# Performance work log

Measured on AMD Instinct MI355X. Metric: run time of the kernel, lower is better.

## Reference

```python
import jax, jax.numpy as jnp
import numpy as np

N_NODES = 50000
N_EDGES = 800000
IN_C = 128
OUT_C = 128
BN_EPS = 1e-5


def setup_inputs() -> dict:
    key = jax.random.key(0)
    k1, k2, k3 = jax.random.split(key, 3)
    x = jax.random.normal(k1, (N_NODES, IN_C), dtype=jnp.float32)
    edge_index = jax.random.randint(k2, (2, N_EDGES), 0, N_NODES, dtype=jnp.int32)
    W = jax.random.normal(k3, (IN_C, OUT_C), dtype=jnp.float32) * (1.0 / np.sqrt(IN_C))
    bias = jnp.zeros((OUT_C,), dtype=jnp.float32)
    gamma = jnp.ones((OUT_C,), dtype=jnp.float32)
    beta = jnp.zeros((OUT_C,), dtype=jnp.float32)
    return {"x": x, "W": W, "bias": bias, "gamma": gamma, "beta": beta,
            "edge_index": edge_index}


def reference(x, W, bias, gamma, beta, edge_index):
    # GCNConv (PyG defaults): add self-loops, symmetric normalization, linear, scatter-add
    n = x.shape[0]
    h = x @ W  # [N, out_c]
    loops = jnp.arange(n, dtype=edge_index.dtype)
    row = jnp.concatenate([edge_index[0], loops])  # source nodes
    col = jnp.concatenate([edge_index[1], loops])  # target nodes
    # degree of targets (with self-loops, so deg >= 1)
    deg = jnp.zeros((n,), dtype=h.dtype).at[col].add(1.0)
    dinv = jax.lax.rsqrt(deg)
    norm = dinv[row] * dinv[col]  # [E+N]
    msg = h[row] * norm[:, None]  # gather + per-edge scale, [E+N, out_c]
    agg = jax.ops.segment_sum(msg, col, num_segments=n) + bias  # scatter-add
    # BatchNorm1d over node dimension (training-mode batch statistics)
    mean = jnp.mean(agg, axis=0)
    var = jnp.var(agg, axis=0)
    y = (agg - mean) * jax.lax.rsqrt(var + BN_EPS) * gamma + beta
    # ReLU; dropout is identity at inference
    return jax.nn.relu(y)
```

## Files before the change

kernel.cpp:

```cpp
#include <hip/hip_runtime.h>

#define N_NODES 50000
#define N_EDGES 800000
#define C 128
#define BN_EPS 1e-5f
#define BSHIFT 7
#define NBUCK ((N_NODES + 127) >> BSHIFT)
#define EPB 2048
#define A_BLOCKS ((N_EDGES + EPB - 1) / EPB)
#define EBUF 2560
#define GEMM_BLOCKS ((N_NODES + 63) / 64)
#define GATHER_BLOCKS 512
#define GATHER_WAVES (GATHER_BLOCKS * 8)

typedef __attribute__((ext_vector_type(8))) short bf16x8;
typedef __attribute__((ext_vector_type(4))) float f32x4;

__device__ __forceinline__ unsigned pack_bf16x2(float a, float b) {
    unsigned ua = __float_as_uint(a);
    ua = (ua + 0x7FFFu + ((ua >> 16) & 1u)) >> 16;
    unsigned ub = __float_as_uint(b);
    ub = (ub + 0x7FFFu + ((ub >> 16) & 1u)) >> 16;
    return ua | (ub << 16);
}

__device__ __forceinline__ unsigned short bf16_1(float a) {
    unsigned u = __float_as_uint(a);
    return (unsigned short)((u + 0x7FFFu + ((u >> 16) & 1u)) >> 16);
}

__device__ __forceinline__ float blo(unsigned u) { return __uint_as_float(u << 16); }
__device__ __forceinline__ float bhi(unsigned u) { return __uint_as_float(u & 0xFFFF0000u); }

__device__ __forceinline__ unsigned pack_f16x2(float a, float b) {
    _Float16 ha = (_Float16)a, hb = (_Float16)b;
    return (unsigned)__builtin_bit_cast(unsigned short, ha) |
           ((unsigned)__builtin_bit_cast(unsigned short, hb) << 16);
}
__device__ __forceinline__ float f16lo(unsigned u) {
    return (float)__builtin_bit_cast(_Float16, (unsigned short)(u & 0xFFFFu));
}
__device__ __forceinline__ float f16hi(unsigned u) {
    return (float)__builtin_bit_cast(_Float16, (unsigned short)(u >> 16));
}

__global__ void __launch_bounds__(256) k_scat(const int* __restrict__ row,
                                              const int* __restrict__ col,
                                              unsigned* __restrict__ bEdges,
                                              int* __restrict__ bOffsT,
                                              const float* __restrict__ W,
                                              unsigned* __restrict__ WTn,
                                              float* __restrict__ sums8) {
    int tid = threadIdx.x, w = blockIdx.x;
    if (w == A_BLOCKS) {
#pragma unroll
        for (int it = 0; it < 32; ++it) {
            int i = tid + (it << 8);
            int j = i & 3, l = (i >> 2) & 63, kt = (i >> 8) & 3, nt = i >> 10;
            int m = l & 15, q = l >> 4;
            int kr = kt * 32 + q * 8 + 2 * j;
            int n = nt * 16 + m;
            WTn[i] = pack_bf16x2(W[kr * C + n], W[(kr + 1) * C + n]);
        }
        for (int i = tid; i < 2048; i += 256) sums8[i] = 0.f;
        return;
    }
    __shared__ int hist[NBUCK];
    __shared__ int wsum[8];
    int lane = tid & 63, wid = tid >> 6;
    for (int i = tid; i < NBUCK; i += 256) hist[i] = 0;
    __syncthreads();
    int e0 = w * EPB;
    int nE = N_EDGES - e0; if (nE > EPB) nE = EPB;
    int myc[8], myr[8];
#pragma unroll
    for (int k = 0; k < 8; ++k) {
        int idx = tid + (k << 8);
        bool ok = idx < nE;
        myc[k] = ok ? col[e0 + idx] : -1;
        myr[k] = ok ? row[e0 + idx] : 0;
        if (ok) atomicAdd(&hist[myc[k] >> BSHIFT], 1);
    }
    __syncthreads();
    int v0 = hist[tid];
    int v1 = (tid + 256 < NBUCK) ? hist[tid + 256] : 0;
    int s0 = v0, s1 = v1;
#pragma unroll
    for (int d = 1; d < 64; d <<= 1) {
        int u0 = __shfl_up(s0, d, 64);
        int u1 = __shfl_up(s1, d, 64);
        if (lane >= d) { s0 += u0; s1 += u1; }
    }
    if (lane == 63) { wsum[wid] = s0; wsum[4 + wid] = s1; }
    __syncthreads();
    int tot0 = wsum[0] + wsum[1] + wsum[2] + wsum[3];
    int p0 = 0, p1 = tot0;
    for (int i = 0; i < wid; ++i) { p0 += wsum[i]; p1 += wsum[4 + i]; }
    int exc0 = p0 + s0 - v0;
    int exc1 = p1 + s1 - v1;
    bOffsT[tid * A_BLOCKS + w] = exc0;
    if (tid + 256 < NBUCK) bOffsT[(tid + 256) * A_BLOCKS + w] = exc1;
    if (tid == 0) bOffsT[NBUCK * A_BLOCKS + w] = nE;
    hist[tid] = exc0;
    if (tid + 256 < NBUCK) hist[tid + 256] = exc1;
    __syncthreads();
#pragma unroll
    for (int k = 0; k < 8; ++k) {
        if (myc[k] >= 0) {
            int b = myc[k] >> BSHIFT;
            int r = atomicAdd(&hist[b], 1);
            bEdges[(size_t)w * EPB + r] = (unsigned)myr[k] | ((unsigned)myc[k] << 16);
        }
    }
}

__global__ void __launch_bounds__(256) k_mid(const unsigned* __restrict__ bEdges,
                                             const int* __restrict__ bOffsT,
                                             int2* __restrict__ nodeDesc,
                                             float* __restrict__ dinvArr,
                                             unsigned short* __restrict__ srcs,
                                             const float* __restrict__ x,
                                             const unsigned* __restrict__ WTn,
                                             unsigned short* __restrict__ g16) {
    __shared__ __align__(16) unsigned sm[4352];
    __shared__ int wsum[12];
    __shared__ int wtot;
    int tid = threadIdx.x;
    int lane = tid & 63, wid = tid >> 6;
    if (blockIdx.x < NBUCK) {
        const int b = blockIdx.x;
        int* sS = (int*)sm;
        int* sO = (int*)sm + 392;
        unsigned* ebuf = sm + 792;
        int* h = (int*)(sm + 792 + EBUF);
        int i1 = tid + 256;
        int st0 = bOffsT[b * A_BLOCKS + tid];
        int v0 = bOffsT[(b + 1) * A_BLOCKS + tid] - st0;
        int st1 = 0, v1 = 0;
        if (i1 < A_BLOCKS) {
            st1 = bOffsT[b * A_BLOCKS + i1];
            v1 = bOffsT[(b + 1) * A_BLOCKS + i1] - st1;
        }
        sS[tid] = st0;
        if (i1 < A_BLOCKS) sS[i1] = st1;
        if (tid < 128) h[tid] = 0;
        int ep = st0 + st1;
        int s0 = v0, s1 = v1;
#pragma unroll
        for (int d = 1; d < 64; d <<= 1) {
            int u0 = __shfl_up(s0, d, 64);
            int u1 = __shfl_up(s1, d, 64);
            if (lane >= d) { s0 += u0; s1 += u1; }
            ep += __shfl_xor(ep, d, 64);
        }
        if (lane == 63) { wsum[wid] = s0; wsum[4 + wid] = s1; }
        if (lane == 0) wsum[8 + wid] = ep;
        __syncthreads();
        int tot0 = wsum[0] + wsum[1] + wsum[2] + wsum[3];
        int tot1 = wsum[4] + wsum[5] + wsum[6] + wsum[7];
        int e0 = wsum[8] + wsum[9] + wsum[10] + wsum[11];
        int p0 = 0, p1 = tot0;
        for (int i = 0; i < wid; ++i) { p0 += wsum[i]; p1 += wsum[4 + i]; }
        sO[tid] = p0 + s0 - v0;
        if (i1 < A_BLOCKS) sO[i1] = p1 + s1 - v1;
        if (tid == 0) sO[A_BLOCKS] = tot0 + tot1;
        __syncthreads();
        int c = sO[A_BLOCKS];
        if (c > EBUF) c = EBUF;
        for (int seg = tid; seg < A_BLOCKS; seg += 256) {
            int o = sO[seg];
            int n = sO[seg + 1] - o;
            const unsigned* srcp = bEdges + (size_t)seg * EPB + sS[seg];
            for (int k = 0; k < n; ++k) {
                int dp = o + k;
                if (dp < EBUF) ebuf[dp] = srcp[k];
            }
        }
        __syncthreads();
        int n0 = b << BSHIFT;
        int nn = N_NODES - n0; if (nn > 128) nn = 128;
        for (int e = tid; e < c; e += 256)
            atomicAdd(&h[(int)(ebuf[e] >> 16) - n0], 1);
        __syncthreads();
        int v = 0, sc = 0;
        if (tid < 128) {
            int ln = tid & 63;
            v = h[tid];
            sc = v;
#pragma unroll
            for (int d = 1; d < 64; d <<= 1) {
                int u = __shfl_up(sc, d, 64);
                if (ln >= d) sc += u;
            }
            if (tid == 63) wtot = sc;
        }
        __syncthreads();
        if (tid < 128) {
            int ex = sc - v + ((tid >= 64) ? wtot : 0);
            if (tid < nn) {
                nodeDesc[n0 + tid] = make_int2(e0 + ex, v);
                dinvArr[n0 + tid] = rsqrtf((float)v + 1.f);
            }
            h[tid] = ex;
        }
        __syncthreads();
        for (int e = tid; e < c; e += 256) {
            unsigned pe = ebuf[e];
            int r = atomicAdd(&h[(int)(pe >> 16) - n0], 1);
            srcs[e0 + r] = (unsigned short)(pe & 0xFFFFu);
        }
    } else {
        unsigned* xs = sm;
        int r0 = (blockIdx.x - NBUCK) * 64;
        const float4* x4 = (const float4*)x;
#pragma unroll
        for (int it = 0; it < 8; ++it) {
            int i = tid + (it << 8);
            int r = i >> 5, c4 = i & 31;
            float4 v = {0.f, 0.f, 0.f, 0.f};
            if (r0 + r < N_NODES) v = x4[(size_t)(r0 + r) * 32 + c4];
            xs[r * 68 + c4 * 2]     = pack_bf16x2(v.x, v.y);
            xs[r * 68 + c4 * 2 + 1] = pack_bf16x2(v.z, v.w);
        }
        __syncthreads();
        int r0w = r0 + wid * 16;
        if (r0w >= N_NODES) return;
        int m = lane & 15, q = lane >> 4;
        bf16x8 afrag[4];
#pragma unroll
        for (int kt = 0; kt < 4; ++kt)
            afrag[kt] = *(const bf16x8*)&xs[(wid * 16 + m) * 68 + kt * 16 + q * 4];
        const uint4* B4 = (const uint4*)WTn;
        f32x4 acc[8];
#pragma unroll
        for (int nt = 0; nt < 8; ++nt)
            acc[nt][0] = acc[nt][1] = acc[nt][2] = acc[nt][3] = 0.f;
#pragma unroll
        for (int nt = 0; nt < 8; ++nt) {
#pragma unroll
            for (int kt = 0; kt < 4; ++kt) {
                uint4 braw = B4[(nt * 4 + kt) * 64 + lane];
                bf16x8 bfrag = __builtin_bit_cast(bf16x8, braw);
                acc[nt] = __builtin_amdgcn_mfma_f32_16x16x32_bf16(afrag[kt], bfrag, acc[nt], 0, 0, 0);
            }
        }
        int rb = r0w + q * 4;
#pragma unroll
        for (int nt = 0; nt < 8; ++nt) {
            int cbase = nt * 16 + m;
#pragma unroll
            for (int reg = 0; reg < 4; ++reg)
                g16[(size_t)(rb + reg) * C + cbase] = bf16_1(acc[nt][reg]);
        }
    }
}

#define ACC8S(v, d) { a[0]+=blo(v.x)*d; a[1]+=bhi(v.x)*d; a[2]+=blo(v.y)*d; a[3]+=bhi(v.y)*d; \
                      a[4]+=blo(v.z)*d; a[5]+=bhi(v.z)*d; a[6]+=blo(v.w)*d; a[7]+=bhi(v.w)*d; }

__device__ __forceinline__ void acc_batch(const uint4* __restrict__ g4, int l, int q,
                                          int sv, float dvv, int nb, float* a) {
    int j0 = 0;
    for (; j0 + 16 <= nb; j0 += 16) {
        int i0 = j0 + q;
        int s0 = __shfl(sv, i0, 64);
        int s1 = __shfl(sv, i0 + 4, 64);
        int s2 = __shfl(sv, i0 + 8, 64);
        int s3 = __shfl(sv, i0 + 12, 64);
        float d0 = __shfl(dvv, i0, 64);
        float d1 = __shfl(dvv, i0 + 4, 64);
        float d2 = __shfl(dvv, i0 + 8, 64);
        float d3 = __shfl(dvv, i0 + 12, 64);
        uint4 v0 = g4[(size_t)s0 * 16 + l];
        uint4 v1 = g4[(size_t)s1 * 16 + l];
        uint4 v2 = g4[(size_t)s2 * 16 + l];
        uint4 v3 = g4[(size_t)s3 * 16 + l];
        ACC8S(v0, d0) ACC8S(v1, d1) ACC8S(v2, d2) ACC8S(v3, d3)
    }
    if (j0 < nb) {
#pragma unroll
        for (int k = 0; k < 4; ++k) {
            int idx = j0 + q + 4 * k;
            int s = __shfl(sv, idx, 64);
            float d = __shfl(dvv, idx, 64);
            if (idx < nb) { uint4 v = g4[(size_t)s * 16 + l]; ACC8S(v, d) }
        }
    }
}

__global__ void __launch_bounds__(512) k_gather(const int2* __restrict__ nodeDesc,
                                                const unsigned short* __restrict__ srcs,
                                                const uint4* __restrict__ g4,
                                                const float* __restrict__ dinvArr,
                                                unsigned* __restrict__ aggh,
                                                float* __restrict__ sums8) {
    __shared__ float lsA[8][32][4], lsQ[8][32][4];
    int tid = threadIdx.x;
    int lane = tid & 63, wid = tid >> 6;
    int l = lane & 15, q = lane >> 4;
    float sA[4] = {0.f, 0.f, 0.f, 0.f}, sQ[4] = {0.f, 0.f, 0.f, 0.f};
    int gw = blockIdx.x * 8 + wid;

    int nA = gw, nB = gw + GATHER_WAVES, nC = gw + 2 * GATHER_WAVES;
    int2 dA = {0, 0}, dB = {0, 0};
    int svA = 0; float dvA = 0.f;
    if (nA < N_NODES) {
        dA = nodeDesc[nA];
        if (lane < dA.y) { svA = srcs[dA.x + lane]; dvA = dinvArr[svA]; }
    }
    if (nB < N_NODES) dB = nodeDesc[nB];

    while (nA < N_NODES) {
        int svB = 0; float dvB = 0.f;
        if (nB < N_NODES && lane < dB.y) { svB = srcs[dB.x + lane]; dvB = dinvArr[svB]; }
        int2 dC = {0, 0};
        if (nC < N_NODES) dC = nodeDesc[nC];

        float dt = rsqrtf((float)dA.y + 1.f);
        float a[8];
        if (q == 0) {
            uint4 u = g4[(size_t)nA * 16 + l];
            a[0]=blo(u.x)*dt; a[1]=bhi(u.x)*dt; a[2]=blo(u.y)*dt; a[3]=bhi(u.y)*dt;
            a[4]=blo(u.z)*dt; a[5]=bhi(u.z)*dt; a[6]=blo(u.w)*dt; a[7]=bhi(u.w)*dt;
        } else {
#pragma unroll
            for (int i = 0; i < 8; ++i) a[i] = 0.f;
        }
        int nb0 = dA.y < 64 ? dA.y : 64;
        acc_batch(g4, l, q, svA, dvA, nb0, a);
        for (int base = dA.x + 64; base < dA.x + dA.y; base += 64) {
            int nb = dA.x + dA.y - base; if (nb > 64) nb = 64;
            int sv2 = 0; float dv2 = 0.f;
            if (lane < nb) { sv2 = srcs[base + lane]; dv2 = dinvArr[sv2]; }
            acc_batch(g4, l, q, sv2, dv2, nb, a);
        }
#pragma unroll
        for (int i = 0; i < 8; ++i) {
            a[i] += __shfl_xor(a[i], 16, 64);
            a[i] += __shfl_xor(a[i], 32, 64);
        }
        if (q < 2) {
            float f0 = a[q * 4 + 0] * dt, f1 = a[q * 4 + 1] * dt;
            float f2 = a[q * 4 + 2] * dt, f3 = a[q * 4 + 3] * dt;
            sA[0] += f0; sQ[0] += f0 * f0;
            sA[1] += f1; sQ[1] += f1 * f1;
            sA[2] += f2; sQ[2] += f2 * f2;
            sA[3] += f3; sQ[3] += f3 * f3;
            uint2 pv; pv.x = pack_f16x2(f0, f1); pv.y = pack_f16x2(f2, f3);
            *(uint2*)(aggh + (size_t)nA * 64 + l * 4 + q * 2) = pv;
        }
        nA = nB; dA = dB; svA = svB; dvA = dvB;
        nB = nC; dB = dC; nC += GATHER_WAVES;
    }

    if (q < 2) {
#pragma unroll
        for (int i = 0; i < 4; ++i) {
            lsA[wid][l * 2 + q][i] = sA[i];
            lsQ[wid][l * 2 + q][i] = sQ[i];
        }
    }
    __syncthreads();
    if (tid < 128) {
        int ll = tid >> 3, qq = (tid >> 2) & 1, ii = tid & 3;
        float s = 0.f, sq = 0.f;
#pragma unroll
        for (int wd = 0; wd < 8; ++wd) {
            s  += lsA[wd][ll * 2 + qq][ii];
            sq += lsQ[wd][ll * 2 + qq][ii];
        }
        int slice = (blockIdx.x & 7) * 256;
        atomicAdd(&sums8[slice + tid], s);
        atomicAdd(&sums8[slice + 128 + tid], sq);
    }
}

__global__ void __launch_bounds__(256) k_final(const unsigned* __restrict__ aggh,
                                               float* __restrict__ out,
                                               const float* __restrict__ sums8,
                                               const float* __restrict__ gamma,
                                               const float* __restrict__ beta) {
    __shared__ float sc_s[C], sh_s[C];
    int tid = threadIdx.x;
    if (tid < C) {
        float s = 0.f, sq = 0.f;
#pragma unroll
        for (int k = 0; k < 8; ++k) {
            s  += sums8[k * 256 + tid];
            sq += sums8[k * 256 + 128 + tid];
        }
        float mean = s * (1.0f / N_NODES);
        float var = sq * (1.0f / N_NODES) - mean * mean;
        float sc = gamma[tid] * rsqrtf(var + BN_EPS);
        sc_s[tid] = sc;
        sh_s[tid] = beta[tid] - mean * sc;
    }
    __syncthreads();
    int i = blockIdx.x * 256 + tid;
    uint4 v = ((const uint4*)aggh)[i];
    int c = (i & 15) * 8;
    float4 o0, o1;
    o0.x = fmaxf(f16lo(v.x) * sc_s[c+0] + sh_s[c+0], 0.f);
    o0.y = fmaxf(f16hi(v.x) * sc_s[c+1] + sh_s[c+1], 0.f);
    o0.z = fmaxf(f16lo(v.y) * sc_s[c+2] + sh_s[c+2], 0.f);
    o0.w = fmaxf(f16hi(v.y) * sc_s[c+3] + sh_s[c+3], 0.f);
    o1.x = fmaxf(f16lo(v.z) * sc_s[c+4] + sh_s[c+4], 0.f);
    o1.y = fmaxf(f16hi(v.z) * sc_s[c+5] + sh_s[c+5], 0.f);
    o1.z = fmaxf(f16lo(v.w) * sc_s[c+6] + sh_s[c+6], 0.f);
    o1.w = fmaxf(f16hi(v.w) * sc_s[c+7] + sh_s[c+7], 0.f);
    float4* o = (float4*)(out + (size_t)i * 8);
    o[0] = o0; o[1] = o1;
}

extern "C" void kernel_launch(void* const* d_in, const int* in_sizes, int n_in,
                              void* d_out, int out_size, void* d_ws, size_t ws_size,
                              hipStream_t stream) {
    const float* x     = (const float*)d_in[0];
    const float* W     = (const float*)d_in[1];
    const float* gamma = (const float*)d_in[3];
    const float* beta  = (const float*)d_in[4];
    const int*   eidx  = (const int*)d_in[5];
    const int* row = eidx;
    const int* col = eidx + N_EDGES;

    float* out = (float*)d_out;

    unsigned* g      = (unsigned*)d_ws;
    unsigned* aggh   = g + (size_t)N_NODES * 64;
    unsigned* bEdges = aggh + (size_t)N_NODES * 64;
    unsigned* WTn    = bEdges + (size_t)A_BLOCKS * EPB;
    unsigned short* srcs = (unsigned short*)(WTn + 8192);
    int2*  nodeDesc = (int2*)(srcs + N_EDGES);
    float* dinvArr  = (float*)(nodeDesc + N_NODES);
    float* sums8    = dinvArr + N_NODES;
    int*   bOffsT   = (int*)(sums8 + 2048);

    k_scat<<<A_BLOCKS + 1, 256, 0, stream>>>(row, col, bEdges, bOffsT, W, WTn, sums8);
    k_mid<<<NBUCK + GEMM_BLOCKS, 256, 0, stream>>>(bEdges, bOffsT, nodeDesc, dinvArr, srcs,
                                                   x, WTn, (unsigned short*)g);
    k_gather<<<GATHER_BLOCKS, 512, 0, stream>>>(nodeDesc, srcs, (const uint4*)g, dinvArr, aggh, sums8);
    k_final<<<N_NODES * 16 / 256, 256, 0, stream>>>(aggh, out, sums8, gamma, beta);
}
```

Baseline: 155.9 us.

## Fuse four kernels into one persistent kernel with software grid barriers

Merges the bucket-scatter, CSR-build/GEMM, gather-aggregate and BatchNorm-apply kernels into a single persistent kernel of 512 blocks. The phases are separated by a global atomic-counter barrier. This removes three kernel launches and their inter-kernel gaps. In exchange, the work loops now stride over units, the gather drops its software prefetch pipeline and runs with 4 waves per block instead of 8, and correctness relies on all 512 blocks being co-resident.

Result: slower. 556.5 us (+257.0%).

```diff
diff --git a/kernel.cpp b/kernel.cpp
--- a/kernel.cpp
+++ b/kernel.cpp
@@ -9,12 +9,27 @@
 #define EPB 2048
 #define A_BLOCKS ((N_EDGES + EPB - 1) / EPB)
 #define EBUF 2560
-#define GEMM_BLOCKS ((N_NODES + 63) / 64)
-#define GATHER_BLOCKS 512
-#define GATHER_WAVES (GATHER_BLOCKS * 8)
+#define GEMM_UNITS ((N_NODES + 63) / 64)
+#define NBLK 512
+#define NTHR 256
+#define GWAVES (NBLK * 4)
 
 typedef __attribute__((ext_vector_type(8))) short bf16x8;
 typedef __attribute__((ext_vector_type(4))) float f32x4;
+
+__device__ unsigned g_bar = 0;
+
+__device__ __forceinline__ void gbarrier() {
+    __threadfence();
+    __syncthreads();
+    if (threadIdx.x == 0) {
+        unsigned a = atomicAdd(&g_bar, 1u);
+        unsigned target = (a / NBLK + 1u) * NBLK;
+        while (atomicAdd(&g_bar, 0u) < target) __builtin_amdgcn_s_sleep(8);
+    }
+    __syncthreads();
+    __threadfence();
+}
 
 __device__ __forceinline__ unsigned pack_bf16x2(float a, float b) {
     unsigned ua = __float_as_uint(a);
@@ -42,217 +57,6 @@
 }
 __device__ __forceinline__ float f16hi(unsigned u) {
     return (float)__builtin_bit_cast(_Float16, (unsigned short)(u >> 16));
-}
-
-__global__ void __launch_bounds__(256) k_scat(const int* __restrict__ row,
-                                              const int* __restrict__ col,
-                                              unsigned* __restrict__ bEdges,
-                                              int* __restrict__ bOffsT,
-                                              const float* __restrict__ W,
-                                              unsigned* __restrict__ WTn,
-                                              float* __restrict__ sums8) {
-    int tid = threadIdx.x, w = blockIdx.x;
-    if (w == A_BLOCKS) {
-#pragma unroll
-        for (int it = 0; it < 32; ++it) {
-            int i = tid + (it << 8);
-            int j = i & 3, l = (i >> 2) & 63, kt = (i >> 8) & 3, nt = i >> 10;
-            int m = l & 15, q = l >> 4;
-            int kr = kt * 32 + q * 8 + 2 * j;
-            int n = nt * 16 + m;
-            WTn[i] = pack_bf16x2(W[kr * C + n], W[(kr + 1) * C + n]);
-        }
-        for (int i = tid; i < 2048; i += 256) sums8[i] = 0.f;
-        return;
-    }
-    __shared__ int hist[NBUCK];
-    __shared__ int wsum[8];
-    int lane = tid & 63, wid = tid >> 6;
-    for (int i = tid; i < NBUCK; i += 256) hist[i] = 0;
-    __syncthreads();
-    int e0 = w * EPB;
-    int nE = N_EDGES - e0; if (nE > EPB) nE = EPB;
-    int myc[8], myr[8];
-#pragma unroll
-    for (int k = 0; k < 8; ++k) {
-        int idx = tid + (k << 8);
-        bool ok = idx < nE;
-        myc[k] = ok ? col[e0 + idx] : -1;
-        myr[k] = ok ? row[e0 + idx] : 0;
-        if (ok) atomicAdd(&hist[myc[k] >> BSHIFT], 1);
-    }
-    __syncthreads();
-    int v0 = hist[tid];
-    int v1 = (tid + 256 < NBUCK) ? hist[tid + 256] : 0;
-    int s0 = v0, s1 = v1;
-#pragma unroll
-    for (int d = 1; d < 64; d <<= 1) {
-        int u0 = __shfl_up(s0, d, 64);
-        int u1 = __shfl_up(s1, d, 64);
-        if (lane >= d) { s0 += u0; s1 += u1; }
-    }
-    if (lane == 63) { wsum[wid] = s0; wsum[4 + wid] = s1; }
-    __syncthreads();
-    int tot0 = wsum[0] + wsum[1] + wsum[2] + wsum[3];
-    int p0 = 0, p1 = tot0;
-    for (int i = 0; i < wid; ++i) { p0 += wsum[i]; p1 += wsum[4 + i]; }
-    int exc0 = p0 + s0 - v0;
-    int exc1 = p1 + s1 - v1;
-    bOffsT[tid * A_BLOCKS + w] = exc0;
-    if (tid + 256 < NBUCK) bOffsT[(tid + 256) * A_BLOCKS + w] = exc1;
-    if (tid == 0) bOffsT[NBUCK * A_BLOCKS + w] = nE;
-    hist[tid] = exc0;
-    if (tid + 256 < NBUCK) hist[tid + 256] = exc1;
-    __syncthreads();
-#pragma unroll
-    for (int k = 0; k < 8; ++k) {
-        if (myc[k] >= 0) {
-            int b = myc[k] >> BSHIFT;
-            int r = atomicAdd(&hist[b], 1);
-            bEdges[(size_t)w * EPB + r] = (unsigned)myr[k] | ((unsigned)myc[k] << 16);
-        }
-    }
-}
-
-__global__ void __launch_bounds__(256) k_mid(const unsigned* __restrict__ bEdges,
-                                             const int* __restrict__ bOffsT,
-                                             int2* __restrict__ nodeDesc,
-                                             float* __restrict__ dinvArr,
-                                             unsigned short* __restrict__ srcs,
-                                             const float* __restrict__ x,
-                                             const unsigned* __restrict__ WTn,
-                                             unsigned short* __restrict__ g16) {
-    __shared__ __align__(16) unsigned sm[4352];
-    __shared__ int wsum[12];
-    __shared__ int wtot;
-    int tid = threadIdx.x;
-    int lane = tid & 63, wid = tid >> 6;
-    if (blockIdx.x < NBUCK) {
-        const int b = blockIdx.x;
-        int* sS = (int*)sm;
-        int* sO = (int*)sm + 392;
-        unsigned* ebuf = sm + 792;
-        int* h = (int*)(sm + 792 + EBUF);
-        int i1 = tid + 256;
-        int st0 = bOffsT[b * A_BLOCKS + tid];
-        int v0 = bOffsT[(b + 1) * A_BLOCKS + tid] - st0;
-        int st1 = 0, v1 = 0;
-        if (i1 < A_BLOCKS) {
-            st1 = bOffsT[b * A_BLOCKS + i1];
-            v1 = bOffsT[(b + 1) * A_BLOCKS + i1] - st1;
-        }
-        sS[tid] = st0;
-        if (i1 < A_BLOCKS) sS[i1] = st1;
-        if (tid < 128) h[tid] = 0;
-        int ep = st0 + st1;
-        int s0 = v0, s1 = v1;
-#pragma unroll
-        for (int d = 1; d < 64; d <<= 1) {
-            int u0 = __shfl_up(s0, d, 64);
-            int u1 = __shfl_up(s1, d, 64);
-            if (lane >= d) { s0 += u0; s1 += u1; }
-            ep += __shfl_xor(ep, d, 64);
-        }
-        if (lane == 63) { wsum[wid] = s0; wsum[4 + wid] = s1; }
-        if (lane == 0) wsum[8 + wid] = ep;
-        __syncthreads();
-        int tot0 = wsum[0] + wsum[1] + wsum[2] + wsum[3];
-        int tot1 = wsum[4] + wsum[5] + wsum[6] + wsum[7];
-        int e0 = wsum[8] + wsum[9] + wsum[10] + wsum[11];
-        int p0 = 0, p1 = tot0;
-        for (int i = 0; i < wid; ++i) { p0 += wsum[i]; p1 += wsum[4 + i]; }
-        sO[tid] = p0 + s0 - v0;
-        if (i1 < A_BLOCKS) sO[i1] = p1 + s1 - v1;
-        if (tid == 0) sO[A_BLOCKS] = tot0 + tot1;
-        __syncthreads();
-        int c = sO[A_BLOCKS];
-        if (c > EBUF) c = EBUF;
-        for (int seg = tid; seg < A_BLOCKS; seg += 256) {
-            int o = sO[seg];
-            int n = sO[seg + 1] - o;
-            const unsigned* srcp = bEdges + (size_t)seg * EPB + sS[seg];
-            for (int k = 0; k < n; ++k) {
-                int dp = o + k;
-                if (dp < EBUF) ebuf[dp] = srcp[k];
-            }
-        }
-        __syncthreads();
-        int n0 = b << BSHIFT;
-        int nn = N_NODES - n0; if (nn > 128) nn = 128;
-        for (int e = tid; e < c; e += 256)
-            atomicAdd(&h[(int)(ebuf[e] >> 16) - n0], 1);
-        __syncthreads();
-        int v = 0, sc = 0;
-        if (tid < 128) {
-            int ln = tid & 63;
-            v = h[tid];
-            sc = v;
-#pragma unroll
-            for (int d = 1; d < 64; d <<= 1) {
-                int u = __shfl_up(sc, d, 64);
-                if (ln >= d) sc += u;
-            }
-            if (tid == 63) wtot = sc;
-        }
-        __syncthreads();
-        if (tid < 128) {
-            int ex = sc - v + ((tid >= 64) ? wtot : 0);
-            if (tid < nn) {
-                nodeDesc[n0 + tid] = make_int2(e0 + ex, v);
-                dinvArr[n0 + tid] = rsqrtf((float)v + 1.f);
-            }
-            h[tid] = ex;
-        }
-        __syncthreads();
-        for (int e = tid; e < c; e += 256) {
-            unsigned pe = ebuf[e];
-            int r = atomicAdd(&h[(int)(pe >> 16) - n0], 1);
-            srcs[e0 + r] = (unsigned short)(pe & 0xFFFFu);
-        }
-    } else {
-        unsigned* xs = sm;
-        int r0 = (blockIdx.x - NBUCK) * 64;
-        const float4* x4 = (const float4*)x;
-#pragma unroll
-        for (int it = 0; it < 8; ++it) {
-            int i = tid + (it << 8);
-            int r = i >> 5, c4 = i & 31;
-            float4 v = {0.f, 0.f, 0.f, 0.f};
-            if (r0 + r < N_NODES) v = x4[(size_t)(r0 + r) * 32 + c4];
-            xs[r * 68 + c4 * 2]     = pack_bf16x2(v.x, v.y);
-            xs[r * 68 + c4 * 2 + 1] = pack_bf16x2(v.z, v.w);
-        }
-        __syncthreads();
-        int r0w = r0 + wid * 16;
-        if (r0w >= N_NODES) return;
-        int m = lane & 15, q = lane >> 4;
-        bf16x8 afrag[4];
-#pragma unroll
-        for (int kt = 0; kt < 4; ++kt)
-            afrag[kt] = *(const bf16x8*)&xs[(wid * 16 + m) * 68 + kt * 16 + q * 4];
-        const uint4* B4 = (const uint4*)WTn;
-        f32x4 acc[8];
-#pragma unroll
-        for (int nt = 0; nt < 8; ++nt)
-            acc[nt][0] = acc[nt][1] = acc[nt][2] = acc[nt][3] = 0.f;
-#pragma unroll
-        for (int nt = 0; nt < 8; ++nt) {
-#pragma unroll
-            for (int kt = 0; kt < 4; ++kt) {
-                uint4 braw = B4[(nt * 4 + kt) * 64 + lane];
-                bf16x8 bfrag = __builtin_bit_cast(bf16x8, braw);
-                acc[nt] = __builtin_amdgcn_mfma_f32_16x16x32_bf16(afrag[kt], bfrag, acc[nt], 0, 0, 0);
-            }
-        }
-        int rb = r0w + q * 4;
-#pragma unroll
-        for (int nt = 0; nt < 8; ++nt) {
-            int cbase = nt * 16 + m;
-#pragma unroll
-            for (int reg = 0; reg < 4; ++reg)
-                g16[(size_t)(rb + reg) * C + cbase] = bf16_1(acc[nt][reg]);
-        }
-    }
 }
 
 #define ACC8S(v, d) { a[0]+=blo(v.x)*d; a[1]+=bhi(v.x)*d; a[2]+=blo(v.y)*d; a[3]+=bhi(v.y)*d; \
@@ -288,128 +92,312 @@
     }
 }
 
-__global__ void __launch_bounds__(512) k_gather(const int2* __restrict__ nodeDesc,
-                                                const unsigned short* __restrict__ srcs,
-                                                const uint4* __restrict__ g4,
-                                                const float* __restrict__ dinvArr,
-                                                unsigned* __restrict__ aggh,
-                                                float* __restrict__ sums8) {
-    __shared__ float lsA[8][32][4], lsQ[8][32][4];
-    int tid = threadIdx.x;
-    int lane = tid & 63, wid = tid >> 6;
-    int l = lane & 15, q = lane >> 4;
-    float sA[4] = {0.f, 0.f, 0.f, 0.f}, sQ[4] = {0.f, 0.f, 0.f, 0.f};
-    int gw = blockIdx.x * 8 + wid;
-
-    int nA = gw, nB = gw + GATHER_WAVES, nC = gw + 2 * GATHER_WAVES;
-    int2 dA = {0, 0}, dB = {0, 0};
-    int svA = 0; float dvA = 0.f;
-    if (nA < N_NODES) {
-        dA = nodeDesc[nA];
-        if (lane < dA.y) { svA = srcs[dA.x + lane]; dvA = dinvArr[svA]; }
-    }
-    if (nB < N_NODES) dB = nodeDesc[nB];
-
-    while (nA < N_NODES) {
-        int svB = 0; float dvB = 0.f;
-        if (nB < N_NODES && lane < dB.y) { svB = srcs[dB.x + lane]; dvB = dinvArr[svB]; }
-        int2 dC = {0, 0};
-        if (nC < N_NODES) dC = nodeDesc[nC];
-
-        float dt = rsqrtf((float)dA.y + 1.f);
-        float a[8];
-        if (q == 0) {
-            uint4 u = g4[(size_t)nA * 16 + l];
-            a[0]=blo(u.x)*dt; a[1]=bhi(u.x)*dt; a[2]=blo(u.y)*dt; a[3]=bhi(u.y)*dt;
-            a[4]=blo(u.z)*dt; a[5]=bhi(u.z)*dt; a[6]=blo(u.w)*dt; a[7]=bhi(u.w)*dt;
+__global__ void __launch_bounds__(NTHR, 4) k_fused(
+        const int* __restrict__ erow, const int* __restrict__ ecol,
+        const float* __restrict__ x, const float* __restrict__ W,
+        const float* __restrict__ gamma, const float* __restrict__ beta,
+        float* __restrict__ out,
+        unsigned* __restrict__ gbuf, unsigned* __restrict__ aggh,
+        unsigned* __restrict__ bEdges, int* __restrict__ bOffsT,
+        unsigned* __restrict__ WTn, unsigned short* __restrict__ srcs,
+        int2* __restrict__ nodeDesc, float* __restrict__ dinvArr,
+        float* __restrict__ sums8) {
+    __shared__ __align__(16) unsigned sm[4352];
+    __shared__ int wsum[16];
+    __shared__ int wtot;
+    const int tid = threadIdx.x, bx = blockIdx.x;
+    const int lane = tid & 63, wid = tid >> 6;
+
+    if (bx < A_BLOCKS) {
+        int* hist = (int*)sm;
+        for (int i = tid; i < NBUCK; i += NTHR) hist[i] = 0;
+        __syncthreads();
+        const int w = bx, e0 = w * EPB;
+        int nE = N_EDGES - e0; if (nE > EPB) nE = EPB;
+        int myc[8], myr[8];
+#pragma unroll
+        for (int k = 0; k < 8; ++k) {
+            int idx = tid + (k << 8);
+            bool ok = idx < nE;
+            myc[k] = ok ? ecol[e0 + idx] : -1;
+            myr[k] = ok ? erow[e0 + idx] : 0;
+            if (ok) atomicAdd(&hist[myc[k] >> BSHIFT], 1);
+        }
+        __syncthreads();
+        int v0 = hist[tid];
+        int v1 = (tid + 256 < NBUCK) ? hist[tid + 256] : 0;
+        int s0 = v0, s1 = v1;
+#pragma unroll
+        for (int d = 1; d < 64; d <<= 1) {
+            int u0 = __shfl_up(s0, d, 64);
+            int u1 = __shfl_up(s1, d, 64);
+            if (lane >= d) { s0 += u0; s1 += u1; }
+        }
+        if (lane == 63) { wsum[wid] = s0; wsum[4 + wid] = s1; }
+        __syncthreads();
+        int tot0 = wsum[0] + wsum[1] + wsum[2] + wsum[3];
+        int p0 = 0, p1 = tot0;
+        for (int i = 0; i < wid; ++i) { p0 += wsum[i]; p1 += wsum[4 + i]; }
+        int exc0 = p0 + s0 - v0;
+        int exc1 = p1 + s1 - v1;
+        bOffsT[tid * A_BLOCKS + w] = exc0;
+        if (tid + 256 < NBUCK) bOffsT[(tid + 256) * A_BLOCKS + w] = exc1;
+        if (tid == 0) bOffsT[NBUCK * A_BLOCKS + w] = nE;
+        hist[tid] = exc0;
+        if (tid + 256 < NBUCK) hist[tid + 256] = exc1;
+        __syncthreads();
+#pragma unroll
+        for (int k = 0; k < 8; ++k) {
+            if (myc[k] >= 0) {
+                int b = myc[k] >> BSHIFT;
+                int r = atomicAdd(&hist[b], 1);
+                bEdges[(size_t)w * EPB + r] = (unsigned)myr[k] | ((unsigned)myc[k] << 16);
+            }
+        }
+    } else if (bx == A_BLOCKS) {
+#pragma unroll
+        for (int it = 0; it < 32; ++it) {
+            int i = tid + (it << 8);
+            int j = i & 3, l = (i >> 2) & 63, kt = (i >> 8) & 3, nt = i >> 10;
+            int m = l & 15, q = l >> 4;
+            int kr = kt * 32 + q * 8 + 2 * j;
+            int n = nt * 16 + m;
+            WTn[i] = pack_bf16x2(W[kr * C + n], W[(kr + 1) * C + n]);
+        }
+        for (int i = tid; i < 2048; i += NTHR) sums8[i] = 0.f;
+    }
+    gbarrier();
+
+    for (int u = bx; u < A_BLOCKS + GEMM_UNITS; u += NBLK) {
+        if (u < NBUCK) {
+            const int b = u;
+            int* sS = (int*)sm;
+            int* sO = (int*)sm + 392;
+            unsigned* ebuf = sm + 792;
+            int* h = (int*)(sm + 792 + EBUF);
+            int i1 = tid + 256;
+            int st0 = bOffsT[b * A_BLOCKS + tid];
+            int v0 = bOffsT[(b + 1) * A_BLOCKS + tid] - st0;
+            int st1 = 0, v1 = 0;
+            if (i1 < A_BLOCKS) {
+                st1 = bOffsT[b * A_BLOCKS + i1];
+                v1 = bOffsT[(b + 1) * A_BLOCKS + i1] - st1;
+            }
+            sS[tid] = st0;
+            if (i1 < A_BLOCKS) sS[i1] = st1;
+            if (tid < 128) h[tid] = 0;
+            int ep = st0 + st1;
+            int s0 = v0, s1 = v1;
+#pragma unroll
+            for (int d = 1; d < 64; d <<= 1) {
+                int u0 = __shfl_up(s0, d, 64);
+                int u1 = __shfl_up(s1, d, 64);
+                if (lane >= d) { s0 += u0; s1 += u1; }
+                ep += __shfl_xor(ep, d, 64);
+            }
+            if (lane == 63) { wsum[wid] = s0; wsum[4 + wid] = s1; }
+            if (lane == 0) wsum[8 + wid] = ep;
+            __syncthreads();
+            int tot0 = wsum[0] + wsum[1] + wsum[2] + wsum[3];
+            int tot1 = wsum[4] + wsum[5] + wsum[6] + wsum[7];
+            int e0 = wsum[8] + wsum[9] + wsum[10] + wsum[11];
+            int p0 = 0, p1 = tot0;
+            for (int i = 0; i < wid; ++i) { p0 += wsum[i]; p1 += wsum[4 + i]; }
+            sO[tid] = p0 + s0 - v0;
+            if (i1 < A_BLOCKS) sO[i1] = p1 + s1 - v1;
+            if (tid == 0) sO[A_BLOCKS] = tot0 + tot1;
+            __syncthreads();
+            int c = sO[A_BLOCKS];
+            if (c > EBUF) c = EBUF;
+            for (int seg = tid; seg < A_BLOCKS; seg += NTHR) {
+                int o = sO[seg];
+                int n = sO[seg + 1] - o;
+                const unsigned* srcp = bEdges + (size_t)seg * EPB + sS[seg];
+                for (int k = 0; k < n; ++k) {
+                    int dp = o + k;
+                    if (dp < EBUF) ebuf[dp] = srcp[k];
+                }
+            }
+            __syncthreads();
+            int n0 = b << BSHIFT;
+            int nn = N_NODES - n0; if (nn > 128) nn = 128;
+            for (int e = tid; e < c; e += NTHR)
+                atomicAdd(&h[(int)(ebuf[e] >> 16) - n0], 1);
+            __syncthreads();
+            int v = 0, sc = 0;
+            if (tid < 128) {
+                int ln = tid & 63;
+                v = h[tid];
+                sc = v;
+#pragma unroll
+                for (int d = 1; d < 64; d <<= 1) {
+                    int uu = __shfl_up(sc, d, 64);
+                    if (ln >= d) sc += uu;
+                }
+                if (tid == 63) wtot = sc;
+            }
+            __syncthreads();
+            if (tid < 128) {
+                int ex = sc - v + ((tid >= 64) ? wtot : 0);
+                if (tid < nn) {
+                    nodeDesc[n0 + tid] = make_int2(e0 + ex, v);
+                    dinvArr[n0 + tid] = rsqrtf((float)v + 1.f);
+                }
+                h[tid] = ex;
+            }
+            __syncthreads();
+            for (int e = tid; e < c; e += NTHR) {
+                unsigned pe = ebuf[e];
+                int r = atomicAdd(&h[(int)(pe >> 16) - n0], 1);
+                srcs[e0 + r] = (unsigned short)(pe & 0xFFFFu);
+            }
         } else {
-#pragma unroll
-            for (int i = 0; i < 8; ++i) a[i] = 0.f;
-        }
-        int nb0 = dA.y < 64 ? dA.y : 64;
-        acc_batch(g4, l, q, svA, dvA, nb0, a);
-        for (int base = dA.x + 64; base < dA.x + dA.y; base += 64) {
-            int nb = dA.x + dA.y - base; if (nb > 64) nb = 64;
-            int sv2 = 0; float dv2 = 0.f;
-            if (lane < nb) { sv2 = srcs[base + lane]; dv2 = dinvArr[sv2]; }
-            acc_batch(g4, l, q, sv2, dv2, nb, a);
-        }
-#pragma unroll
-        for (int i = 0; i < 8; ++i) {
-            a[i] += __shfl_xor(a[i], 16, 64);
-            a[i] += __shfl_xor(a[i], 32, 64);
+            unsigned* xs = sm;
+            int r0 = (u - NBUCK) * 64;
+            const float4* x4 = (const float4*)x;
+#pragma unroll
+            for (int it = 0; it < 8; ++it) {
+                int i = tid + (it << 8);
+                int r = i >> 5, c4 = i & 31;
+                float4 v = {0.f, 0.f, 0.f, 0.f};
+                if (r0 + r < N_NODES) v = x4[(size_t)(r0 + r) * 32 + c4];
+                xs[r * 68 + c4 * 2]     = pack_bf16x2(v.x, v.y);
+                xs[r * 68 + c4 * 2 + 1] = pack_bf16x2(v.z, v.w);
+            }
+            __syncthreads();
+            int r0w = r0 + wid * 16;
+            if (r0w < N_NODES) {
+                int m = lane & 15, q = lane >> 4;
+                bf16x8 afrag[4];
+#pragma unroll
+                for (int kt = 0; kt < 4; ++kt)
+                    afrag[kt] = *(const bf16x8*)&xs[(wid * 16 + m) * 68 + kt * 16 + q * 4];
+                const uint4* B4 = (const uint4*)WTn;
+                f32x4 acc[8];
+#pragma unroll
+                for (int nt = 0; nt < 8; ++nt)
+                    acc[nt][0] = acc[nt][1] = acc[nt][2] = acc[nt][3] = 0.f;
+#pragma unroll
+                for (int nt = 0; nt < 8; ++nt) {
+#pragma unroll
+                    for (int kt = 0; kt < 4; ++kt) {
+                        uint4 braw = B4[(nt * 4 + kt) * 64 + lane];
+                        bf16x8 bfrag = __builtin_bit_cast(bf16x8, braw);
+                        acc[nt] = __builtin_amdgcn_mfma_f32_16x16x32_bf16(afrag[kt], bfrag, acc[nt], 0, 0, 0);
+                    }
+                }
+                unsigned short* g16 = (unsigned short*)gbuf;
+                int rb = r0w + q * 4;
+#pragma unroll
+                for (int nt = 0; nt < 8; ++nt) {
+                    int cbase = nt * 16 + m;
+#pragma unroll
+                    for (int reg = 0; reg < 4; ++reg)
+                        g16[(size_t)(rb + reg) * C + cbase] = bf16_1(acc[nt][reg]);
+                }
+            }
+        }
+        __syncthreads();
+    }
+    gbarrier();
+
+    {
+        float* lsA = (float*)sm;
+        float* lsQ = lsA + 512;
+        const uint4* g4 = (const uint4*)gbuf;
+        const int l = lane & 15, q = lane >> 4;
+        float sA[4] = {0.f, 0.f, 0.f, 0.f}, sQ[4] = {0.f, 0.f, 0.f, 0.f};
+        for (int node = bx * 4 + wid; node < N_NODES; node += GWAVES) {
+            int2 d = nodeDesc[node];
+            int beg = d.x, deg = d.y;
+            float dt = rsqrtf((float)deg + 1.f);
+            float a[8];
+            if (q == 0) {
+                uint4 u = g4[(size_t)node * 16 + l];
+                a[0]=blo(u.x)*dt; a[1]=bhi(u.x)*dt; a[2]=blo(u.y)*dt; a[3]=bhi(u.y)*dt;
+                a[4]=blo(u.z)*dt; a[5]=bhi(u.z)*dt; a[6]=blo(u.w)*dt; a[7]=bhi(u.w)*dt;
+            } else {
+#pragma unroll
+                for (int i = 0; i < 8; ++i) a[i] = 0.f;
+            }
+            for (int base = beg; base < beg + deg; base += 64) {
+                int nb = beg + deg - base; if (nb > 64) nb = 64;
+                int sv = 0; float dvv = 0.f;
+                if (lane < nb) { sv = srcs[base + lane]; dvv = dinvArr[sv]; }
+                acc_batch(g4, l, q, sv, dvv, nb, a);
+            }
+#pragma unroll
+            for (int i = 0; i < 8; ++i) {
+                a[i] += __shfl_xor(a[i], 16, 64);
+                a[i] += __shfl_xor(a[i], 32, 64);
+            }
+            if (q < 2) {
+                float f0 = a[q * 4 + 0] * dt, f1 = a[q * 4 + 1] * dt;
+                float f2 = a[q * 4 + 2] * dt, f3 = a[q * 4 + 3] * dt;
+                sA[0] += f0; sQ[0] += f0 * f0;
+                sA[1] += f1; sQ[1] += f1 * f1;
+                sA[2] += f2; sQ[2] += f2 * f2;
+                sA[3] += f3; sQ[3] += f3 * f3;
+                uint2 pv; pv.x = pack_f16x2(f0, f1); pv.y = pack_f16x2(f2, f3);
+                *(uint2*)(aggh + (size_t)node * 64 + l * 4 + q * 2) = pv;
+            }
         }
         if (q < 2) {
-            float f0 = a[q * 4 + 0] * dt, f1 = a[q * 4 + 1] * dt;
-            float f2 = a[q * 4 + 2] * dt, f3 = a[q * 4 + 3] * dt;
-            sA[0] += f0; sQ[0] += f0 * f0;
-            sA[1] += f1; sQ[1] += f1 * f1;
-            sA[2] += f2; sQ[2] += f2 * f2;
-            sA[3] += f3; sQ[3] += f3 * f3;
-            uint2 pv; pv.x = pack_f16x2(f0, f1); pv.y = pack_f16x2(f2, f3);
-            *(uint2*)(aggh + (size_t)nA * 64 + l * 4 + q * 2) = pv;
-        }
-        nA = nB; dA = dB; svA = svB; dvA = dvB;
-        nB = nC; dB = dC; nC += GATHER_WAVES;
-    }
-
-    if (q < 2) {
-#pragma unroll
-        for (int i = 0; i < 4; ++i) {
-            lsA[wid][l * 2 + q][i] = sA[i];
-            lsQ[wid][l * 2 + q][i] = sQ[i];
-        }
-    }
-    __syncthreads();
-    if (tid < 128) {
-        int ll = tid >> 3, qq = (tid >> 2) & 1, ii = tid & 3;
-        float s = 0.f, sq = 0.f;
-#pragma unroll
-        for (int wd = 0; wd < 8; ++wd) {
-            s  += lsA[wd][ll * 2 + qq][ii];
-            sq += lsQ[wd][ll * 2 + qq][ii];
-        }
-        int slice = (blockIdx.x & 7) * 256;
-        atomicAdd(&sums8[slice + tid], s);
-        atomicAdd(&sums8[slice + 128 + tid], sq);
-    }
-}
-
-__global__ void __launch_bounds__(256) k_final(const unsigned* __restrict__ aggh,
-                                               float* __restrict__ out,
-                                               const float* __restrict__ sums8,
-                                               const float* __restrict__ gamma,
-                                               const float* __restrict__ beta) {
-    __shared__ float sc_s[C], sh_s[C];
-    int tid = threadIdx.x;
-    if (tid < C) {
-        float s = 0.f, sq = 0.f;
-#pragma unroll
-        for (int k = 0; k < 8; ++k) {
-            s  += sums8[k * 256 + tid];
-            sq += sums8[k * 256 + 128 + tid];
-        }
-        float mean = s * (1.0f / N_NODES);
-        float var = sq * (1.0f / N_NODES) - mean * mean;
-        float sc = gamma[tid] * rsqrtf(var + BN_EPS);
-        sc_s[tid] = sc;
-        sh_s[tid] = beta[tid] - mean * sc;
-    }
-    __syncthreads();
-    int i = blockIdx.x * 256 + tid;
-    uint4 v = ((const uint4*)aggh)[i];
-    int c = (i & 15) * 8;
-    float4 o0, o1;
-    o0.x = fmaxf(f16lo(v.x) * sc_s[c+0] + sh_s[c+0], 0.f);
-    o0.y = fmaxf(f16hi(v.x) * sc_s[c+1] + sh_s[c+1], 0.f);
-    o0.z = fmaxf(f16lo(v.y) * sc_s[c+2] + sh_s[c+2], 0.f);
-    o0.w = fmaxf(f16hi(v.y) * sc_s[c+3] + sh_s[c+3], 0.f);
-    o1.x = fmaxf(f16lo(v.z) * sc_s[c+4] + sh_s[c+4], 0.f);
-    o1.y = fmaxf(f16hi(v.z) * sc_s[c+5] + sh_s[c+5], 0.f);
-    o1.z = fmaxf(f16lo(v.w) * sc_s[c+6] + sh_s[c+6], 0.f);
-    o1.w = fmaxf(f16hi(v.w) * sc_s[c+7] + sh_s[c+7], 0.f);
-    float4* o = (float4*)(out + (size_t)i * 8);
-    o[0] = o0; o[1] = o1;
+#pragma unroll
+            for (int i = 0; i < 4; ++i) {
+                lsA[wid * 128 + (l * 2 + q) * 4 + i] = sA[i];
+                lsQ[wid * 128 + (l * 2 + q) * 4 + i] = sQ[i];
+            }
+        }
+        __syncthreads();
+        if (tid < 128) {
+            float s = 0.f, sq = 0.f;
+#pragma unroll
+            for (int wd = 0; wd < 4; ++wd) {
+                s  += lsA[wd * 128 + tid];
+                sq += lsQ[wd * 128 + tid];
+            }
+            int slice = (bx & 7) * 256;
+            atomicAdd(&sums8[slice + tid], s);
+            atomicAdd(&sums8[slice + 128 + tid], sq);
+        }
+    }
+    gbarrier();
+
+    {
+        float* scs = (float*)sm;
+        float* shs = scs + 128;
+        if (tid < C) {
+            float s = 0.f, sq = 0.f;
+#pragma unroll
+            for (int k = 0; k < 8; ++k) {
+                s  += sums8[k * 256 + tid];
+                sq += sums8[k * 256 + 128 + tid];
+            }
+            float mean = s * (1.0f / N_NODES);
+            float var = sq * (1.0f / N_NODES) - mean * mean;
+            float sc = gamma[tid] * rsqrtf(var + BN_EPS);
+            scs[tid] = sc;
+            shs[tid] = beta[tid] - mean * sc;
+        }
+        __syncthreads();
+        const uint4* a4 = (const uint4*)aggh;
+        for (int i = bx * NTHR + tid; i < N_NODES * 16; i += NBLK * NTHR) {
+            uint4 v = a4[i];
+            int c = (i & 15) * 8;
+            float4 o0, o1;
+            o0.x = fmaxf(f16lo(v.x) * scs[c+0] + shs[c+0], 0.f);
+            o0.y = fmaxf(f16hi(v.x) * scs[c+1] + shs[c+1], 0.f);
+            o0.z = fmaxf(f16lo(v.y) * scs[c+2] + shs[c+2], 0.f);
+            o0.w = fmaxf(f16hi(v.y) * scs[c+3] + shs[c+3], 0.f);
+            o1.x = fmaxf(f16lo(v.z) * scs[c+4] + shs[c+4], 0.f);
+            o1.y = fmaxf(f16hi(v.z) * scs[c+5] + shs[c+5], 0.f);
+            o1.z = fmaxf(f16lo(v.w) * scs[c+6] + shs[c+6], 0.f);
+            o1.w = fmaxf(f16hi(v.w) * scs[c+7] + shs[c+7], 0.f);
+            float4* o = (float4*)(out + (size_t)i * 8);
+            o[0] = o0; o[1] = o1;
+        }
+    }
 }
 
 extern "C" void kernel_launch(void* const* d_in, const int* in_sizes, int n_in,
@@ -420,13 +408,13 @@
     const float* gamma = (const float*)d_in[3];
     const float* beta  = (const float*)d_in[4];
     const int*   eidx  = (const int*)d_in[5];
-    const int* row = eidx;
-    const int* col = eidx + N_EDGES;
+    const int* erow = eidx;
+    const int* ecol = eidx + N_EDGES;
 
     float* out = (float*)d_out;
 
-    unsigned* g      = (unsigned*)d_ws;
-    unsigned* aggh   = g + (size_t)N_NODES * 64;
+    unsigned* gbuf   = (unsigned*)d_ws;
+    unsigned* aggh   = gbuf + (size_t)N_NODES * 64;
     unsigned* bEdges = aggh + (size_t)N_NODES * 64;
     unsigned* WTn    = bEdges + (size_t)A_BLOCKS * EPB;
     unsigned short* srcs = (unsigned short*)(WTn + 8192);
@@ -435,9 +423,7 @@
     float* sums8    = dinvArr + N_NODES;
     int*   bOffsT   = (int*)(sums8 + 2048);
 
-    k_scat<<<A_BLOCKS + 1, 256, 0, stream>>>(row, col, bEdges, bOffsT, W, WTn, sums8);
-    k_mid<<<NBUCK + GEMM_BLOCKS, 256, 0, stream>>>(bEdges, bOffsT, nodeDesc, dinvArr, srcs,
-                                                   x, WTn, (unsigned short*)g);
-    k_gather<<<GATHER_BLOCKS, 512, 0, stream>>>(nodeDesc, srcs, (const uint4*)g, dinvArr, aggh, sums8);
-    k_final<<<N_NODES * 16 / 256, 256, 0, stream>>>(aggh, out, sums8, gamma, beta);
-}
+    k_fused<<<NBLK, NTHR, 0, stream>>>(erow, ecol, x, W, gamma, beta, out,
+                                       gbuf, aggh, bEdges, bOffsT, WTn, srcs,
+                                       nodeDesc, dinvArr, sums8);
+}
```
